# Kernel optimization log

Measured on AMD Instinct MI355X. Metric: run time of the kernel, lower is better.

The kernel has to match this reference:

```python
import jax, jax.numpy as jnp
import numpy as np

HEADS = 10
DIM_HEAD = 64
C = 640
N_TOK = 1024          # (1024//32)**2 tokens per image
IMG_NUMS = 3          # total_length = id_length + 1
ID_LENGTH = 2
SA = 0.5
NEG_INF = -1e9


def _build_story_mask(key):
    # Faithful to cal_attn_mask_xl: one random row of columns shared by all
    # images, columns beyond the id_length reference images zeroed, and each
    # image's own block forced True; then broadcast over query tokens.
    L = IMG_NUMS * N_TOK
    base = jax.random.uniform(key, (1, L)) < SA                  # [1, L]
    bm = jnp.tile(base, (IMG_NUMS, 1))                           # [img, L]
    col = jnp.arange(L)
    bm = jnp.where(col[None, :] >= ID_LENGTH * N_TOK, False, bm)
    self_block = (col // N_TOK)[None, :] == jnp.arange(IMG_NUMS)[:, None]
    bm = bm | self_block                                         # [img, L]
    return jnp.repeat(bm, N_TOK, axis=0)                         # [L, L]


def setup_inputs() -> dict:
    key = jax.random.key(0)
    ks = jax.random.split(key, 7)
    B_total = 2 * IMG_NUMS
    hidden_states = jax.random.normal(ks[0], (B_total, N_TOK, C), dtype=jnp.float32)
    mask = _build_story_mask(ks[1])
    s = 1.0 / np.sqrt(C)
    Wq = jax.random.normal(ks[2], (C, HEADS * DIM_HEAD), dtype=jnp.float32) * s
    Wk = jax.random.normal(ks[3], (C, HEADS * DIM_HEAD), dtype=jnp.float32) * s
    Wv = jax.random.normal(ks[4], (C, HEADS * DIM_HEAD), dtype=jnp.float32) * s
    Wout = jax.random.normal(ks[5], (HEADS * DIM_HEAD, C), dtype=jnp.float32) * s
    bout = jnp.zeros((C,), dtype=jnp.float32)
    return {"hidden_states": hidden_states, "mask": mask,
            "Wq": Wq, "Wk": Wk, "Wv": Wv, "Wout": Wout, "bout": bout}


def reference(hidden_states, mask, Wq, Wk, Wv, Wout, bout):
    # __call1__ with encoder_hidden_states=None: fuse img_nums images into one
    # long sequence per CFG branch, then masked SDPA.
    B_total, n_tok, c = hidden_states.shape
    img_nums = B_total // 2
    L = img_nums * n_tok
    x = hidden_states.reshape(2, L, c)                       # [2, L, C]

    q = jnp.einsum('bsc,cd->bsd', x, Wq).reshape(2, L, HEADS, DIM_HEAD)
    k = jnp.einsum('bsc,cd->bsd', x, Wk).reshape(2, L, HEADS, DIM_HEAD)
    v = jnp.einsum('bsc,cd->bsd', x, Wv).reshape(2, L, HEADS, DIM_HEAD)

    scale = 1.0 / jnp.sqrt(jnp.asarray(DIM_HEAD, dtype=q.dtype))
    scores = jnp.einsum('bqhd,bkhd->bhqk', q, k) * scale     # [2, H, L, L]
    scores = jnp.where(mask[None, None, :, :], scores, NEG_INF)
    attn = jax.nn.softmax(scores, axis=-1)
    out = jnp.einsum('bhqk,bkhd->bqhd', attn, v)             # [2, L, H, Dh]
    out = out.reshape(B_total, n_tok, HEADS * DIM_HEAD)
    return jnp.einsum('bsd,dc->bsc', out, Wout) + bout
```

## Files before the change

kernel.cpp:

```cpp
#include <hip/hip_runtime.h>
#include <cstdint>
#include <cstddef>

typedef _Float16 f16;
typedef _Float16 f16x8 __attribute__((ext_vector_type(8)));
typedef _Float16 f16x4 __attribute__((ext_vector_type(4)));
typedef float f32x4 __attribute__((ext_vector_type(4)));

#define MFMA32(a, b, c) __builtin_amdgcn_mfma_f32_16x16x32_f16((a), (b), (c), 0, 0, 0)
#define MFMA16(a, b, c) __builtin_amdgcn_mfma_f32_16x16x16f16((a), (b), (c), 0, 0, 0)

#if __has_builtin(__builtin_amdgcn_exp2f)
#define EXP2F(x) __builtin_amdgcn_exp2f(x)
#else
#define EXP2F(x) exp2f(x)
#endif

#define LOG2E 1.44269504088896340736f

#define WAIT_VM4_BAR() asm volatile("s_waitcnt vmcnt(4) lgkmcnt(0)\n\ts_barrier" ::: "memory")
#define WAIT_VM0_BAR() asm volatile("s_waitcnt vmcnt(0) lgkmcnt(0)\n\ts_barrier" ::: "memory")
#define WAIT_LGKM_BAR() asm volatile("s_waitcnt lgkmcnt(0)\n\ts_barrier" ::: "memory")

__device__ __forceinline__ f16x4 pack4(float a, float b, float c, float d) {
    f16x4 r; r[0] = (f16)a; r[1] = (f16)b; r[2] = (f16)c; r[3] = (f16)d;
    return r;
}

__device__ __forceinline__ void gl_lds16(const f16* g, f16* l) {
    __builtin_amdgcn_global_load_lds((const __attribute__((address_space(1))) void*)g,
                                     (__attribute__((address_space(3))) void*)l, 16, 0, 0);
}

__global__ __launch_bounds__(256) void k_cvt_x(const float4* __restrict__ x, f16x4* __restrict__ xb) {
    const int i = blockIdx.x * 256 + threadIdx.x;
    const float4 v = x[i];
    f16x4 o;
    o[0] = (f16)v.x; o[1] = (f16)v.y; o[2] = (f16)v.z; o[3] = (f16)v.w;
    xb[i] = o;
}

__global__ __launch_bounds__(256) void k_cvt_w(const float* __restrict__ Wq, const float* __restrict__ Wk,
                                               const float* __restrict__ Wv, const float* __restrict__ Wo,
                                               f16* __restrict__ WT, f16* __restrict__ WoT) {
    __shared__ float tile[32][33];
    const int z = blockIdx.z;
    const float* src = (z == 0) ? Wq : (z == 1) ? Wk : (z == 2) ? Wv : Wo;
    f16* dst = (z < 3) ? (WT + (size_t)z * 640 * 640) : WoT;
    const float scale = (z == 0) ? 0.125f * LOG2E : 1.0f;
    const int k0 = blockIdx.x * 32, n0 = blockIdx.y * 32;
    const int t = threadIdx.x;
#pragma unroll
    for (int i = 0; i < 4; i++) {
        const int idx = i * 256 + t;
        const int r = idx >> 5, c = idx & 31;
        tile[r][c] = src[(size_t)(k0 + r) * 640 + n0 + c];
    }
    __syncthreads();
#pragma unroll
    for (int i = 0; i < 4; i++) {
        const int idx = i * 256 + t;
        const int r = idx >> 5, c = idx & 31;
        dst[(size_t)(n0 + r) * 640 + k0 + c] = (f16)(tile[c][r] * scale);
    }
}

__global__ __launch_bounds__(256) void k_bias(const unsigned char* __restrict__ mask,
                                              float* __restrict__ biasg) {
    const int idx = blockIdx.x * 256 + threadIdx.x;
    const int img = idx / 3072, col = idx - img * 3072;
    int mmode;
    if (mask[1] && mask[2] && mask[3]) mmode = 0;
    else if (mask[7] == 0x3f) mmode = 2;
    else mmode = 1;
    const int msz = (mmode == 0) ? 1 : 4;
    const int mhi = (mmode == 2) ? 3 : 0;
    biasg[idx] = (mask[((size_t)img * 1024 * 3072 + col) * msz + mhi] != 0) ? -8.f : -1e9f;
}

__global__ __launch_bounds__(256) void k_gemm(const f16* __restrict__ A, const f16* __restrict__ B,
                                              f16* __restrict__ qb, f16* __restrict__ kb, f16* __restrict__ vtb) {
    __shared__ f16 As[128 * 40];
    __shared__ f16 Bs[128 * 40];
    const int t = threadIdx.x;
    const int wave = t >> 6, lane = t & 63, quad = lane >> 4, l16 = lane & 15;
    const int wm = wave >> 1, wn = wave & 1;
    const long m0 = (long)blockIdx.x * 128, n0 = (long)blockIdx.y * 128;
    const int srow = t >> 2, skc = t & 3;

    const f32x4 zero = {0.f, 0.f, 0.f, 0.f};
    f32x4 acc[4][4];
#pragma unroll
    for (int i = 0; i < 4; i++)
#pragma unroll
        for (int j = 0; j < 4; j++) acc[i][j] = zero;

    const f16* gA1 = A + (m0 + srow) * 640 + skc * 8;
    const f16* gA2 = A + (m0 + 64 + srow) * 640 + skc * 8;
    const f16* gB1 = B + (n0 + srow) * 640 + skc * 8;
    const f16* gB2 = B + (n0 + 64 + srow) * 640 + skc * 8;
    f16* sA1 = As + srow * 40 + skc * 8;
    f16* sA2 = As + (64 + srow) * 40 + skc * 8;
    f16* sB1 = Bs + srow * 40 + skc * 8;
    f16* sB2 = Bs + (64 + srow) * 40 + skc * 8;

    for (int kt = 0; kt < 20; kt++) {
        const int ko = kt * 32;
        const f16x8 a1 = *(const f16x8*)(gA1 + ko);
        const f16x8 a2 = *(const f16x8*)(gA2 + ko);
        const f16x8 b1 = *(const f16x8*)(gB1 + ko);
        const f16x8 b2 = *(const f16x8*)(gB2 + ko);
        __syncthreads();
        *(f16x8*)sA1 = a1;
        *(f16x8*)sA2 = a2;
        *(f16x8*)sB1 = b1;
        *(f16x8*)sB2 = b2;
        __syncthreads();
        f16x8 af[4], bfr[4];
#pragma unroll
        for (int mi = 0; mi < 4; mi++) af[mi] = *(const f16x8*)(As + (wm * 64 + mi * 16 + l16) * 40 + quad * 8);
#pragma unroll
        for (int ni = 0; ni < 4; ni++) bfr[ni] = *(const f16x8*)(Bs + (wn * 64 + ni * 16 + l16) * 40 + quad * 8);
#pragma unroll
        for (int mi = 0; mi < 4; mi++)
#pragma unroll
            for (int ni = 0; ni < 4; ni++) acc[mi][ni] = MFMA32(af[mi], bfr[ni], acc[mi][ni]);
    }

    const int b = (int)(m0 / 3072);
    const int which = (int)(n0 / 640);
    const int hd0 = (int)(n0 - (long)which * 640);
    if (which < 2) {
        f16* dst = (which == 0) ? qb : kb;
#pragma unroll
        for (int ni = 0; ni < 4; ni++) {
            const int hd = hd0 + wn * 64 + ni * 16 + l16;
            const int h = hd >> 6, d = hd & 63;
#pragma unroll
            for (int mi = 0; mi < 4; mi++) {
                const long l0 = m0 - (long)b * 3072 + wm * 64 + mi * 16 + quad * 4;
                f16* p = dst + ((long)(b * 10 + h) * 3072 + l0) * 64 + d;
#pragma unroll
                for (int j = 0; j < 4; j++) p[(long)j * 64] = (f16)acc[mi][ni][j];
            }
        }
    } else {
#pragma unroll
        for (int ni = 0; ni < 4; ni++) {
            const int hd = hd0 + wn * 64 + ni * 16 + l16;
            const int h = hd >> 6, d = hd & 63;
#pragma unroll
            for (int mi = 0; mi < 4; mi++) {
                const long l0 = m0 - (long)b * 3072 + wm * 64 + mi * 16 + quad * 4;
                const long col = (l0 & ~63L) + quad * 16 + mi * 4;
                f16x4 tmp;
#pragma unroll
                for (int j = 0; j < 4; j++) tmp[j] = (f16)acc[mi][ni][j];
                *(f16x4*)(vtb + ((size_t)(b * 10 + h) * 64 + d) * 3072 + col) = tmp;
            }
        }
    }
}

__global__ __launch_bounds__(256) void k_gemmo(const f16* __restrict__ A, const f16* __restrict__ B,
                                               float* __restrict__ out, const float* __restrict__ bias) {
    __shared__ f16 As[64 * 40];
    __shared__ f16 Bs[128 * 40];
    const int t = threadIdx.x;
    const int wave = t >> 6, lane = t & 63, quad = lane >> 4, l16 = lane & 15;
    const int wm = wave >> 1, wn = wave & 1;
    const long m0 = (long)blockIdx.x * 64, n0 = (long)blockIdx.y * 128;
    const int srow = t >> 2, skc = t & 3;

    const f32x4 zero = {0.f, 0.f, 0.f, 0.f};
    f32x4 acc[2][4];
#pragma unroll
    for (int i = 0; i < 2; i++)
#pragma unroll
        for (int j = 0; j < 4; j++) acc[i][j] = zero;

    const f16* gA = A + (m0 + srow) * 640 + skc * 8;
    const f16* gB1 = B + (n0 + srow) * 640 + skc * 8;
    const f16* gB2 = B + (n0 + 64 + srow) * 640 + skc * 8;
    f16* sA = As + srow * 40 + skc * 8;
    f16* sB1 = Bs + srow * 40 + skc * 8;
    f16* sB2 = Bs + (64 + srow) * 40 + skc * 8;

    for (int kt = 0; kt < 20; kt++) {
        const int ko = kt * 32;
        const f16x8 a1 = *(const f16x8*)(gA + ko);
        const f16x8 b1 = *(const f16x8*)(gB1 + ko);
        const f16x8 b2 = *(const f16x8*)(gB2 + ko);
        __syncthreads();
        *(f16x8*)sA = a1;
        *(f16x8*)sB1 = b1;
        *(f16x8*)sB2 = b2;
        __syncthreads();
        f16x8 af[2], bfr[4];
#pragma unroll
        for (int mi = 0; mi < 2; mi++) af[mi] = *(const f16x8*)(As + (wm * 32 + mi * 16 + l16) * 40 + quad * 8);
#pragma unroll
        for (int ni = 0; ni < 4; ni++) bfr[ni] = *(const f16x8*)(Bs + (wn * 64 + ni * 16 + l16) * 40 + quad * 8);
#pragma unroll
        for (int mi = 0; mi < 2; mi++)
#pragma unroll
            for (int ni = 0; ni < 4; ni++) acc[mi][ni] = MFMA32(af[mi], bfr[ni], acc[mi][ni]);
    }

#pragma unroll
    for (int ni = 0; ni < 4; ni++) {
        const long gc = n0 + wn * 64 + ni * 16 + l16;
        const float bs = bias[gc];
#pragma unroll
        for (int mi = 0; mi < 2; mi++) {
            const long r0 = m0 + wm * 32 + mi * 16 + quad * 4;
            float* p = out + r0 * 640 + gc;
#pragma unroll
            for (int j = 0; j < 4; j++) p[(long)j * 640] = acc[mi][ni][j] + bs;
        }
    }
}

__global__ __launch_bounds__(256, 4) void k_attn(const f16* __restrict__ q, const f16* __restrict__ k,
                                                 const f16* __restrict__ vT, const float* __restrict__ biasg,
                                                 f16* __restrict__ Op, float* __restrict__ lp) {
    __shared__ __align__(16) unsigned char smem[38912];

    const int t = threadIdx.x;
    const int w = t >> 6, lane = t & 63, quad = lane >> 4, l16 = lane & 15;
    const int bh = blockIdx.y, b = bh / 10, h = bh - b * 10;

    const int qt = (int)blockIdx.x >> 1;
    const int s = (int)blockIdx.x & 1;
    const int q0 = qt * 128;
    const int img = qt >> 3;
    const int kk0 = (img == 2) ? s * 1536 : s * 1024;
    const int nIter = (img == 2) ? 24 : 16;
    float* bias_s = (float*)(smem + 32768);

    {
        const float* bg = biasg + img * 3072 + kk0;
        for (int i = t; i < nIter * 64; i += 256) bias_s[i] = bg[i];
    }

    const int r8 = lane >> 3, cch = lane & 7;
    const f16* kg = k + (size_t)bh * 3072 * 64;
    const f16* vg = vT + (size_t)bh * 64 * 3072;
    const int wrow0 = w * 16;

#pragma unroll
    for (int pt = 0; pt < 2; pt++) {
        const int k0p = kk0 + (pt << 6);
        f16* Kp = (f16*)(smem + pt * 8192);
        f16* Vp = (f16*)(smem + 16384 + pt * 8192);
#pragma unroll
        for (int i = 0; i < 2; i++) {
            const int row = wrow0 + i * 8 + r8;
            gl_lds16(kg + (size_t)(k0p + row) * 64 + ((cch ^ (row & 7)) * 8), Kp + (wrow0 + i * 8) * 64);
            gl_lds16(vg + (size_t)row * 3072 + k0p + ((cch ^ (row & 7)) * 8), Vp + (wrow0 + i * 8) * 64);
        }
    }

    f16x8 qfA0, qfA1, qfB0, qfB1;
    {
        const f16* qp = q + ((size_t)bh * 3072 + q0 + w * 32 + l16) * 64 + quad * 8;
        qfA0 = *(const f16x8*)qp;
        qfA1 = *(const f16x8*)(qp + 32);
        qfB0 = *(const f16x8*)(qp + 16 * 64);
        qfB1 = *(const f16x8*)(qp + 16 * 64 + 32);
    }

    const int s7 = l16 & 7;
    const int bK0 = l16 * 128 + ((quad ^ s7) * 16);
    const int bK1 = l16 * 128 + (((quad + 4) ^ s7) * 16);
    const int bV0 = l16 * 128 + (((2 * quad) ^ s7) * 16);
    const int bV1 = l16 * 128 + (((2 * quad + 1) ^ s7) * 16);

    const f32x4 zero = {0.f, 0.f, 0.f, 0.f};
    f32x4 OA[4], OB[4];
#pragma unroll
    for (int i = 0; i < 4; i++) { OA[i] = zero; OB[i] = zero; }
    float lA = 0.f, lB = 0.f;

    for (int it = 0; it < nIter; it++) {
        if (it + 1 < nIter) WAIT_VM4_BAR();
        else                WAIT_VM0_BAR();

        const char* Kb = (const char*)smem + (it & 1) * 8192;
        const char* Vb = (const char*)smem + 16384 + (it & 1) * 8192;

        f32x4 bv[4];
#pragma unroll
        for (int kt = 0; kt < 4; kt++) bv[kt] = *(const f32x4*)(bias_s + it * 64 + kt * 16 + quad * 4);

        f32x4 sA[4], sB[4];
#pragma unroll
        for (int kt = 0; kt < 4; kt++) {
            const f16x8 kf0 = *(const f16x8*)(Kb + bK0 + kt * 2048);
            const f16x8 kf1 = *(const f16x8*)(Kb + bK1 + kt * 2048);
            sA[kt] = MFMA32(kf0, qfA0, zero);
            sA[kt] = MFMA32(kf1, qfA1, sA[kt]);
            sB[kt] = MFMA32(kf0, qfB0, zero);
            sB[kt] = MFMA32(kf1, qfB1, sB[kt]);
        }
#pragma unroll
        for (int kt = 0; kt < 4; kt++) {
            sA[kt] += bv[kt];
            sB[kt] += bv[kt];
        }

        f16x4 pkA[4], pkB[4];
#pragma unroll
        for (int kt = 0; kt < 4; kt++) {
            const float a0 = EXP2F(sA[kt][0]), a1 = EXP2F(sA[kt][1]);
            const float a2 = EXP2F(sA[kt][2]), a3 = EXP2F(sA[kt][3]);
            lA += (a0 + a1) + (a2 + a3);
            pkA[kt] = pack4(a0, a1, a2, a3);
            const float b0 = EXP2F(sB[kt][0]), b1 = EXP2F(sB[kt][1]);
            const float b2 = EXP2F(sB[kt][2]), b3 = EXP2F(sB[kt][3]);
            lB += (b0 + b1) + (b2 + b3);
            pkB[kt] = pack4(b0, b1, b2, b3);
        }

#pragma unroll
        for (int mtd = 0; mtd < 4; mtd++) {
            const f16x8 v80 = *(const f16x8*)(Vb + bV0 + mtd * 2048);
            const f16x8 v81 = *(const f16x8*)(Vb + bV1 + mtd * 2048);
            const f16x4 vf0 = __builtin_shufflevector(v80, v80, 0, 1, 2, 3);
            const f16x4 vf1 = __builtin_shufflevector(v80, v80, 4, 5, 6, 7);
            const f16x4 vf2 = __builtin_shufflevector(v81, v81, 0, 1, 2, 3);
            const f16x4 vf3 = __builtin_shufflevector(v81, v81, 4, 5, 6, 7);
            OA[mtd] = MFMA16(vf0, pkA[0], OA[mtd]);
            OA[mtd] = MFMA16(vf1, pkA[1], OA[mtd]);
            OA[mtd] = MFMA16(vf2, pkA[2], OA[mtd]);
            OA[mtd] = MFMA16(vf3, pkA[3], OA[mtd]);
            OB[mtd] = MFMA16(vf0, pkB[0], OB[mtd]);
            OB[mtd] = MFMA16(vf1, pkB[1], OB[mtd]);
            OB[mtd] = MFMA16(vf2, pkB[2], OB[mtd]);
            OB[mtd] = MFMA16(vf3, pkB[3], OB[mtd]);
        }

        WAIT_LGKM_BAR();
        if (it + 2 < nIter) {
            const int k0n = kk0 + ((it + 2) << 6);
            f16* Kn = (f16*)(smem + (it & 1) * 8192);
            f16* Vn = (f16*)(smem + 16384 + (it & 1) * 8192);
#pragma unroll
            for (int i = 0; i < 2; i++) {
                const int row = wrow0 + i * 8 + r8;
                gl_lds16(kg + (size_t)(k0n + row) * 64 + ((cch ^ (row & 7)) * 8), Kn + (wrow0 + i * 8) * 64);
                gl_lds16(vg + (size_t)row * 3072 + k0n + ((cch ^ (row & 7)) * 8), Vn + (wrow0 + i * 8) * 64);
            }
        }
    }

    lA += __shfl_xor(lA, 16);
    lA += __shfl_xor(lA, 32);
    lB += __shfl_xor(lB, 16);
    lB += __shfl_xor(lB, 32);
    const float invA = (lA > 0.f) ? 1.0f / lA : 0.f;
    const float invB = (lB > 0.f) ? 1.0f / lB : 0.f;
    const int rowA = b * 3072 + q0 + w * 32 + l16;
    f16* orowA = Op + (size_t)s * 6144 * 640 + (size_t)rowA * 640 + h * 64;
    f16* orowB = orowA + (size_t)16 * 640;
#pragma unroll
    for (int mtd = 0; mtd < 4; mtd++) {
        f16x4 oa, ob;
#pragma unroll
        for (int j = 0; j < 4; j++) { oa[j] = (f16)(OA[mtd][j] * invA); ob[j] = (f16)(OB[mtd][j] * invB); }
        *(f16x4*)(orowA + mtd * 16 + quad * 4) = oa;
        *(f16x4*)(orowB + mtd * 16 + quad * 4) = ob;
    }
    if (quad == 0) lp[((size_t)s * 6144 + rowA) * 10 + h] = lA;
    if (quad == 1) lp[((size_t)s * 6144 + rowA + 16) * 10 + h] = lB;
}

__global__ __launch_bounds__(256) void k_comb(const f16* __restrict__ Op, const float* __restrict__ lp,
                                              f16* __restrict__ ao) {
    const int idx = blockIdx.x * 256 + threadIdx.x;
    const int row = idx / 80;
    const int c8 = (idx - row * 80) * 8;
    const int h = c8 >> 6;
    float acc[8] = {0.f, 0.f, 0.f, 0.f, 0.f, 0.f, 0.f, 0.f};
    float lsum = 0.f;
#pragma unroll
    for (int s = 0; s < 2; s++) {
        const float l = lp[((size_t)s * 6144 + row) * 10 + h];
        const f16x8 o = *(const f16x8*)(Op + ((size_t)s * 6144 + row) * 640 + c8);
#pragma unroll
        for (int j = 0; j < 8; j++) acc[j] += l * (float)o[j];
        lsum += l;
    }
    const float inv = 1.0f / lsum;
    f16x8 r;
#pragma unroll
    for (int j = 0; j < 8; j++) r[j] = (f16)(acc[j] * inv);
    *(f16x8*)(ao + (size_t)row * 640 + c8) = r;
}

extern "C" void kernel_launch(void* const* d_in, const int* in_sizes, int n_in,
                              void* d_out, int out_size, void* d_ws, size_t ws_size,
                              hipStream_t stream) {
    (void)in_sizes; (void)n_in; (void)out_size; (void)ws_size;
    const float* x = (const float*)d_in[0];
    const unsigned char* mask = (const unsigned char*)d_in[1];
    const float* Wq = (const float*)d_in[2];
    const float* Wk = (const float*)d_in[3];
    const float* Wv = (const float*)d_in[4];
    const float* Wo = (const float*)d_in[5];
    const float* bout = (const float*)d_in[6];
    float* out = (float*)d_out;

    f16* xb  = (f16*)d_ws;
    f16* WT  = xb + 6144 * 640;
    f16* WoT = WT + 1920 * 640;
    f16* qb  = WoT + 640 * 640;
    f16* kb  = qb + 20 * 3072 * 64;
    f16* vtb = kb + 20 * 3072 * 64;
    f16* Op  = vtb + 20 * 3072 * 64;
    float* lp = (float*)(Op + (size_t)2 * 6144 * 640);
    float* biasg = lp + (size_t)2 * 6144 * 10;

    k_cvt_x<<<3840, 256, 0, stream>>>((const float4*)x, (f16x4*)xb);
    k_cvt_w<<<dim3(20, 20, 4), 256, 0, stream>>>(Wq, Wk, Wv, Wo, WT, WoT);
    k_bias<<<36, 256, 0, stream>>>(mask, biasg);
    k_gemm<<<dim3(48, 15), 256, 0, stream>>>(xb, WT, qb, kb, vtb);
    k_attn<<<dim3(48, 20), 256, 0, stream>>>(qb, kb, vtb, biasg, Op, lp);
    k_comb<<<1920, 256, 0, stream>>>(Op, lp, qb );
    k_gemmo<<<dim3(96, 5), 256, 0, stream>>>(qb, WoT, out, bout);
}
```

Baseline: 214.7 us.

## Double-buffer GEMM LDS tiles with direct global-to-LDS loads and XOR swizzle

Both projection GEMMs now stage A/B tiles straight into LDS through a gl_lds16 helper, with two buffers so that the load for step k+2 is in flight while step k computes. The LDS layout switches from padded rows to an XOR-swizzled 32-wide layout to avoid bank conflicts. The output GEMM also moves to 128x128 tiles, which halves its grid. This relies on vmcnt-based waits that assume a fixed count of outstanding loads, and the larger tiles mean fewer blocks and more registers per thread.

```diff
diff --git a/kernel.cpp b/kernel.cpp
--- a/kernel.cpp
+++ b/kernel.cpp
@@ -78,15 +78,23 @@
     biasg[idx] = (mask[((size_t)img * 1024 * 3072 + col) * msz + mhi] != 0) ? -8.f : -1e9f;
 }
 
+__device__ __forceinline__ void stage_gemm(const f16* __restrict__ g, int ko, f16* l, int w, int lane) {
+    const int r16 = lane >> 2, cch = lane & 3;
+#pragma unroll
+    for (int i = 0; i < 2; i++) {
+        const int row = w * 32 + i * 16 + r16;
+        gl_lds16(g + (size_t)row * 640 + ko + ((cch ^ (row & 3)) * 8), l + (w * 32 + i * 16) * 32);
+    }
+}
+
 __global__ __launch_bounds__(256) void k_gemm(const f16* __restrict__ A, const f16* __restrict__ B,
                                               f16* __restrict__ qb, f16* __restrict__ kb, f16* __restrict__ vtb) {
-    __shared__ f16 As[128 * 40];
-    __shared__ f16 Bs[128 * 40];
+    __shared__ __align__(16) f16 As[2][128 * 32];
+    __shared__ __align__(16) f16 Bs[2][128 * 32];
     const int t = threadIdx.x;
     const int wave = t >> 6, lane = t & 63, quad = lane >> 4, l16 = lane & 15;
     const int wm = wave >> 1, wn = wave & 1;
     const long m0 = (long)blockIdx.x * 128, n0 = (long)blockIdx.y * 128;
-    const int srow = t >> 2, skc = t & 3;
 
     const f32x4 zero = {0.f, 0.f, 0.f, 0.f};
     f32x4 acc[4][4];
@@ -95,36 +103,39 @@
 #pragma unroll
         for (int j = 0; j < 4; j++) acc[i][j] = zero;
 
-    const f16* gA1 = A + (m0 + srow) * 640 + skc * 8;
-    const f16* gA2 = A + (m0 + 64 + srow) * 640 + skc * 8;
-    const f16* gB1 = B + (n0 + srow) * 640 + skc * 8;
-    const f16* gB2 = B + (n0 + 64 + srow) * 640 + skc * 8;
-    f16* sA1 = As + srow * 40 + skc * 8;
-    f16* sA2 = As + (64 + srow) * 40 + skc * 8;
-    f16* sB1 = Bs + srow * 40 + skc * 8;
-    f16* sB2 = Bs + (64 + srow) * 40 + skc * 8;
+    const f16* Ag = A + m0 * 640;
+    const f16* Bg = B + n0 * 640;
+
+    stage_gemm(Ag, 0, As[0], wave, lane);
+    stage_gemm(Bg, 0, Bs[0], wave, lane);
+    stage_gemm(Ag, 32, As[1], wave, lane);
+    stage_gemm(Bg, 32, Bs[1], wave, lane);
+
+    const int sw = (quad ^ (l16 & 3)) * 16;
+    const int baseA = (wm * 64 + l16) * 64 + sw;
+    const int baseB = (wn * 64 + l16) * 64 + sw;
 
     for (int kt = 0; kt < 20; kt++) {
-        const int ko = kt * 32;
-        const f16x8 a1 = *(const f16x8*)(gA1 + ko);
-        const f16x8 a2 = *(const f16x8*)(gA2 + ko);
-        const f16x8 b1 = *(const f16x8*)(gB1 + ko);
-        const f16x8 b2 = *(const f16x8*)(gB2 + ko);
-        __syncthreads();
-        *(f16x8*)sA1 = a1;
-        *(f16x8*)sA2 = a2;
-        *(f16x8*)sB1 = b1;
-        *(f16x8*)sB2 = b2;
-        __syncthreads();
+        if (kt + 1 < 20) WAIT_VM4_BAR();
+        else             WAIT_VM0_BAR();
+
+        const char* Asb = (const char*)As[kt & 1];
+        const char* Bsb = (const char*)Bs[kt & 1];
         f16x8 af[4], bfr[4];
 #pragma unroll
-        for (int mi = 0; mi < 4; mi++) af[mi] = *(const f16x8*)(As + (wm * 64 + mi * 16 + l16) * 40 + quad * 8);
-#pragma unroll
-        for (int ni = 0; ni < 4; ni++) bfr[ni] = *(const f16x8*)(Bs + (wn * 64 + ni * 16 + l16) * 40 + quad * 8);
+        for (int mi = 0; mi < 4; mi++) af[mi] = *(const f16x8*)(Asb + baseA + mi * 1024);
+#pragma unroll
+        for (int ni = 0; ni < 4; ni++) bfr[ni] = *(const f16x8*)(Bsb + baseB + ni * 1024);
 #pragma unroll
         for (int mi = 0; mi < 4; mi++)
 #pragma unroll
             for (int ni = 0; ni < 4; ni++) acc[mi][ni] = MFMA32(af[mi], bfr[ni], acc[mi][ni]);
+
+        WAIT_LGKM_BAR();
+        if (kt + 2 < 20) {
+            stage_gemm(Ag, (kt + 2) * 32, As[kt & 1], wave, lane);
+            stage_gemm(Bg, (kt + 2) * 32, Bs[kt & 1], wave, lane);
+        }
     }
 
     const int b = (int)(m0 / 3072);
@@ -164,47 +175,53 @@
 
 __global__ __launch_bounds__(256) void k_gemmo(const f16* __restrict__ A, const f16* __restrict__ B,
                                                float* __restrict__ out, const float* __restrict__ bias) {
-    __shared__ f16 As[64 * 40];
-    __shared__ f16 Bs[128 * 40];
+    __shared__ __align__(16) f16 As[2][128 * 32];
+    __shared__ __align__(16) f16 Bs[2][128 * 32];
     const int t = threadIdx.x;
     const int wave = t >> 6, lane = t & 63, quad = lane >> 4, l16 = lane & 15;
     const int wm = wave >> 1, wn = wave & 1;
-    const long m0 = (long)blockIdx.x * 64, n0 = (long)blockIdx.y * 128;
-    const int srow = t >> 2, skc = t & 3;
+    const long m0 = (long)blockIdx.x * 128, n0 = (long)blockIdx.y * 128;
 
     const f32x4 zero = {0.f, 0.f, 0.f, 0.f};
-    f32x4 acc[2][4];
-#pragma unroll
-    for (int i = 0; i < 2; i++)
+    f32x4 acc[4][4];
+#pragma unroll
+    for (int i = 0; i < 4; i++)
 #pragma unroll
         for (int j = 0; j < 4; j++) acc[i][j] = zero;
 
-    const f16* gA = A + (m0 + srow) * 640 + skc * 8;
-    const f16* gB1 = B + (n0 + srow) * 640 + skc * 8;
-    const f16* gB2 = B + (n0 + 64 + srow) * 640 + skc * 8;
-    f16* sA = As + srow * 40 + skc * 8;
-    f16* sB1 = Bs + srow * 40 + skc * 8;
-    f16* sB2 = Bs + (64 + srow) * 40 + skc * 8;
+    const f16* Ag = A + m0 * 640;
+    const f16* Bg = B + n0 * 640;
+
+    stage_gemm(Ag, 0, As[0], wave, lane);
+    stage_gemm(Bg, 0, Bs[0], wave, lane);
+    stage_gemm(Ag, 32, As[1], wave, lane);
+    stage_gemm(Bg, 32, Bs[1], wave, lane);
+
+    const int sw = (quad ^ (l16 & 3)) * 16;
+    const int baseA = (wm * 64 + l16) * 64 + sw;
+    const int baseB = (wn * 64 + l16) * 64 + sw;
 
     for (int kt = 0; kt < 20; kt++) {
-        const int ko = kt * 32;
-        const f16x8 a1 = *(const f16x8*)(gA + ko);
-        const f16x8 b1 = *(const f16x8*)(gB1 + ko);
-        const f16x8 b2 = *(const f16x8*)(gB2 + ko);
-        __syncthreads();
-        *(f16x8*)sA = a1;
-        *(f16x8*)sB1 = b1;
-        *(f16x8*)sB2 = b2;
-        __syncthreads();
-        f16x8 af[2], bfr[4];
-#pragma unroll
-        for (int mi = 0; mi < 2; mi++) af[mi] = *(const f16x8*)(As + (wm * 32 + mi * 16 + l16) * 40 + quad * 8);
-#pragma unroll
-        for (int ni = 0; ni < 4; ni++) bfr[ni] = *(const f16x8*)(Bs + (wn * 64 + ni * 16 + l16) * 40 + quad * 8);
-#pragma unroll
-        for (int mi = 0; mi < 2; mi++)
+        if (kt + 1 < 20) WAIT_VM4_BAR();
+        else             WAIT_VM0_BAR();
+
+        const char* Asb = (const char*)As[kt & 1];
+        const char* Bsb = (const char*)Bs[kt & 1];
+        f16x8 af[4], bfr[4];
+#pragma unroll
+        for (int mi = 0; mi < 4; mi++) af[mi] = *(const f16x8*)(Asb + baseA + mi * 1024);
+#pragma unroll
+        for (int ni = 0; ni < 4; ni++) bfr[ni] = *(const f16x8*)(Bsb + baseB + ni * 1024);
+#pragma unroll
+        for (int mi = 0; mi < 4; mi++)
 #pragma unroll
             for (int ni = 0; ni < 4; ni++) acc[mi][ni] = MFMA32(af[mi], bfr[ni], acc[mi][ni]);
+
+        WAIT_LGKM_BAR();
+        if (kt + 2 < 20) {
+            stage_gemm(Ag, (kt + 2) * 32, As[kt & 1], wave, lane);
+            stage_gemm(Bg, (kt + 2) * 32, Bs[kt & 1], wave, lane);
+        }
     }
 
 #pragma unroll
@@ -212,8 +229,8 @@
         const long gc = n0 + wn * 64 + ni * 16 + l16;
         const float bs = bias[gc];
 #pragma unroll
-        for (int mi = 0; mi < 2; mi++) {
-            const long r0 = m0 + wm * 32 + mi * 16 + quad * 4;
+        for (int mi = 0; mi < 4; mi++) {
+            const long r0 = m0 + wm * 64 + mi * 16 + quad * 4;
             float* p = out + r0 * 640 + gc;
 #pragma unroll
             for (int j = 0; j < 4; j++) p[(long)j * 640] = acc[mi][ni][j] + bs;
@@ -427,5 +444,5 @@
     k_gemm<<<dim3(48, 15), 256, 0, stream>>>(xb, WT, qb, kb, vtb);
     k_attn<<<dim3(48, 20), 256, 0, stream>>>(qb, kb, vtb, biasg, Op, lp);
     k_comb<<<1920, 256, 0, stream>>>(Op, lp, qb );
-    k_gemmo<<<dim3(96, 5), 256, 0, stream>>>(qb, WoT, out, bout);
-}
+    k_gemmo<<<dim3(48, 5), 256, 0, stream>>>(qb, WoT, out, bout);
+}
```

Measured after the change: 211.3 us. No clear change (-1.6%).
